# Optimization experiments

Hardware: AMD Instinct MI355X
Metric: run time of the kernel (lower is better)

Reference implementation:

```python
import jax, jax.numpy as jnp
import numpy as np

N_NODES = 100000
N_EDGES = 1600000
DIM_IN = 128
DIM_OUT = 128


def setup_inputs() -> dict:
    key = jax.random.key(0)
    k1, k2, k3, k4, k5 = jax.random.split(key, 5)
    x = jax.random.normal(k1, (N_NODES, DIM_IN), dtype=jnp.float32)
    W = jax.random.normal(k2, (DIM_OUT, DIM_IN), dtype=jnp.float32) * (1.0 / np.sqrt(DIM_IN))
    vals = jax.random.uniform(k3, (N_EDGES,), dtype=jnp.float32)
    src = jax.random.randint(k4, (N_EDGES,), 0, N_NODES, dtype=jnp.int32)
    dst = jax.random.randint(k5, (N_EDGES,), 0, N_NODES, dtype=jnp.int32)
    return {"x": x, "W": W, "vals": vals, "src": src, "dst": dst}


def reference(x, W, vals, src, dst):
    # Linear projection (nn.Linear with bias=False): h = x @ W^T  -> [N, dim_out]
    h = jnp.einsum('nd,od->no', x, W)
    # Sparse adjacency SpMM in COO form: out[i] = sum_{e: dst[e]==i} vals[e] * h[src[e]]
    msgs = vals[:, None] * h[src]  # [E, dim_out] irregular gather
    out = jax.ops.segment_sum(msgs, dst, num_segments=N_NODES)  # [N, dim_out] scatter-add
    return out
```

## Files before the change

kernel.cpp:

```cpp
#include <hip/hip_runtime.h>

#define N_NODES 100000
#define N_EDGES 1600000
#define DIM 128

#define NPB 64
#define NBUCK 1563
#define EPB 2048
#define NBLK_E 782
#define NBLK_G 1563

#define OFF_H       0
#define OFF_BCNT    25600000
#define OFF_BBASE   25606272
#define OFF_BCUR    25612544
#define OFF_EPACK   25618816
#define OFF_ROWPTR  38418816
#define WS_NEED     38818944

typedef __attribute__((ext_vector_type(8))) __bf16 bf16x8;
typedef __attribute__((ext_vector_type(4))) float  f32x4;

union U4B8 { uint4 u; bf16x8 v; };
union S8B8 { unsigned short s[8]; bf16x8 v; };

static __device__ __forceinline__ unsigned short f2bf(float f) {
    union { float f; unsigned u; } a; a.f = f;
    unsigned r = a.u + 0x7fffu + ((a.u >> 16) & 1u);
    return (unsigned short)(r >> 16);
}

static __device__ __forceinline__ float bf2f(unsigned short h) {
    return __uint_as_float((unsigned)h << 16);
}

static __device__ __forceinline__ float bflo(unsigned b) {
    return __uint_as_float(b << 16);
}
static __device__ __forceinline__ float bfhi(unsigned b) {
    return __uint_as_float(b & 0xffff0000u);
}

__global__ __launch_bounds__(256) void zero_out_kernel(float4* __restrict__ out) {
    int i = blockIdx.x * 256 + threadIdx.x;
    if (i < N_NODES * DIM / 4) out[i] = make_float4(0.f, 0.f, 0.f, 0.f);
}

__global__ __launch_bounds__(256) void zero_bcnt_kernel(int* __restrict__ c) {
    int i = blockIdx.x * 256 + threadIdx.x;
    if (i < NBUCK) c[i] = 0;
}

#define GMR 64
__global__ __launch_bounds__(256) void gemm_mfma_kernel(
        const float4* __restrict__ x4,
        const float4* __restrict__ W4,
        unsigned short* __restrict__ hb16)
{
    __shared__ alignas(16) unsigned whi[128 * 64];
    __shared__ alignas(16) unsigned wlo[128 * 64];

    const int t    = threadIdx.x;
    const int lane = t & 63;
    const int w    = t >> 6;
    const int r0   = blockIdx.x * GMR;

#pragma unroll
    for (int i = 0; i < 16; ++i) {
        int idx = t + 256 * i;
        int j   = idx >> 5;
        int c4  = idx & 31;
        float4 v = W4[idx];
        unsigned short hx = f2bf(v.x), hy = f2bf(v.y);
        unsigned short hz = f2bf(v.z), hw = f2bf(v.w);
        unsigned short lx = f2bf(v.x - bf2f(hx));
        unsigned short ly = f2bf(v.y - bf2f(hy));
        unsigned short lz = f2bf(v.z - bf2f(hz));
        unsigned short lw = f2bf(v.w - bf2f(hw));
        int d = c4 * 2;
        int p = d ^ ((j & 7) << 2);
        int base = j * 64;
        whi[base + p]     = (unsigned)hx | ((unsigned)hy << 16);
        whi[base + p + 1] = (unsigned)hz | ((unsigned)hw << 16);
        wlo[base + p]     = (unsigned)lx | ((unsigned)ly << 16);
        wlo[base + p + 1] = (unsigned)lz | ((unsigned)lw << 16);
    }
    __syncthreads();

    const int arow = r0 + (w << 4) + (lane & 15);
    const bool rok = arow < N_NODES;
    const int kg   = lane >> 4;

    f32x4 acc[8];
#pragma unroll
    for (int jt = 0; jt < 8; ++jt) acc[jt] = (f32x4)(0.f);

#pragma unroll
    for (int ks = 0; ks < 4; ++ks) {
        float4 a0 = make_float4(0.f, 0.f, 0.f, 0.f);
        float4 a1 = make_float4(0.f, 0.f, 0.f, 0.f);
        if (rok) {
            a0 = x4[(size_t)arow * 32 + ks * 8 + kg * 2];
            a1 = x4[(size_t)arow * 32 + ks * 8 + kg * 2 + 1];
        }
        float av[8] = {a0.x, a0.y, a0.z, a0.w, a1.x, a1.y, a1.z, a1.w};
        S8B8 ahi, alo;
#pragma unroll
        for (int e = 0; e < 8; ++e) {
            unsigned short h = f2bf(av[e]);
            ahi.s[e] = h;
            alo.s[e] = f2bf(av[e] - bf2f(h));
        }

        const int d0 = (ks << 4) + (kg << 2);
#pragma unroll
        for (int jt = 0; jt < 8; ++jt) {
            int j  = (jt << 4) + (lane & 15);
            int p0 = d0 ^ ((j & 7) << 2);
            U4B8 bh, bl;
            bh.u = *(const uint4*)&whi[j * 64 + p0];
            bl.u = *(const uint4*)&wlo[j * 64 + p0];
            acc[jt] = __builtin_amdgcn_mfma_f32_16x16x32_bf16(ahi.v, bh.v, acc[jt], 0, 0, 0);
            acc[jt] = __builtin_amdgcn_mfma_f32_16x16x32_bf16(alo.v, bh.v, acc[jt], 0, 0, 0);
            acc[jt] = __builtin_amdgcn_mfma_f32_16x16x32_bf16(ahi.v, bl.v, acc[jt], 0, 0, 0);
        }
    }

#pragma unroll
    for (int jt = 0; jt < 8; ++jt) {
#pragma unroll
        for (int r = 0; r < 4; ++r) {
            int node = r0 + (w << 4) + kg * 4 + r;
            if (node < N_NODES)
                hb16[(size_t)node * 128 + (jt << 4) + (lane & 15)] = f2bf(acc[jt][r]);
        }
    }
}

__global__ __launch_bounds__(256) void bucket_hist_kernel(
        const int* __restrict__ dst, int* __restrict__ bcnt)
{
    __shared__ int lh[NBUCK];
    const int t = threadIdx.x;
    const int e0 = blockIdx.x * EPB;

    for (int i = t; i < NBUCK; i += 256) lh[i] = 0;
    __syncthreads();
#pragma unroll
    for (int r = 0; r < 8; ++r) {
        int e = e0 + (r << 8) + t;
        if (e < N_EDGES) atomicAdd(&lh[dst[e] >> 6], 1);
    }
    __syncthreads();
    const int phase = (blockIdx.x * 613) % NBUCK;
    for (int k = t; k < NBUCK; k += 256) {
        int i = k + phase; if (i >= NBUCK) i -= NBUCK;
        int c = lh[i];
        if (c) atomicAdd(&bcnt[i], c);
    }
}

__global__ __launch_bounds__(256) void bucket_scan_kernel(
        const int* __restrict__ bcnt, int* __restrict__ bbase,
        int* __restrict__ bcur)
{
    __shared__ int wsh[4];
    const int t = threadIdx.x, lane = t & 63, wv = t >> 6;
    int c[8]; int s = 0;
#pragma unroll
    for (int i = 0; i < 8; ++i) {
        int idx = t * 8 + i;
        c[i] = (idx < NBUCK) ? bcnt[idx] : 0;
        s += c[i];
    }
    int v = s;
#pragma unroll
    for (int off = 1; off < 64; off <<= 1) {
        int u = __shfl_up(v, off, 64);
        if (lane >= off) v += u;
    }
    if (lane == 63) wsh[wv] = v;
    __syncthreads();
    int we = 0;
#pragma unroll
    for (int w = 0; w < 4; ++w) we += (w < wv) ? wsh[w] : 0;
    int run = we + (v - s);
#pragma unroll
    for (int i = 0; i < 8; ++i) {
        int idx = t * 8 + i;
        if (idx < NBUCK) { bbase[idx] = run; bcur[idx] = run; }
        run += c[i];
    }
    if (t == 0) bbase[NBUCK] = N_EDGES;
}

__global__ __launch_bounds__(256) void bucket_fill_kernel(
        const int* __restrict__ src, const int* __restrict__ dst,
        const float* __restrict__ vals,
        int* __restrict__ bcur, uint2* __restrict__ ep)
{
    __shared__ int lh[NBUCK];
    __shared__ int lbase[NBUCK];
    const int t = threadIdx.x;
    const int e0 = blockIdx.x * EPB;

    for (int i = t; i < NBUCK; i += 256) lh[i] = 0;
    __syncthreads();
#pragma unroll
    for (int r = 0; r < 8; ++r) {
        int e = e0 + (r << 8) + t;
        if (e < N_EDGES) atomicAdd(&lh[dst[e] >> 6], 1);
    }
    __syncthreads();
    const int phase = (blockIdx.x * 613) % NBUCK;
    for (int k = t; k < NBUCK; k += 256) {
        int i = k + phase; if (i >= NBUCK) i -= NBUCK;
        int c = lh[i];
        lbase[i] = c ? atomicAdd(&bcur[i], c) : 0;
        lh[i] = 0;
    }
    __syncthreads();
#pragma unroll
    for (int r = 0; r < 8; ++r) {
        int e = e0 + (r << 8) + t;
        if (e < N_EDGES) {
            int d  = dst[e];
            int bk = d >> 6;
            int p  = lbase[bk] + atomicAdd(&lh[bk], 1);
            ep[p] = make_uint2((unsigned)src[e] | ((unsigned)(d & 63) << 17),
                               __float_as_uint(vals[e]));
        }
    }
}

__global__ __launch_bounds__(256) void reorder_kernel(
        const int* __restrict__ bbase,
        uint2* __restrict__ ep,
        int* __restrict__ row_ptr)
{
    __shared__ int lcnt[NPB];
    const int t = threadIdx.x;
    const int lane = t & 63;
    const int wv = t >> 6;
    const int b = blockIdx.x;

    const int jb = bbase[b];
    const int je = bbase[b + 1];
    const int cnt = je - jb;

    uint2 e[8];
#pragma unroll
    for (int r = 0; r < 8; ++r) {
        int idx = t + (r << 8);
        if (idx < cnt) e[r] = ep[jb + idx];
    }
    if (t < NPB) lcnt[t] = 0;
    __syncthreads();
#pragma unroll
    for (int r = 0; r < 8; ++r) {
        int idx = t + (r << 8);
        if (idx < cnt) atomicAdd(&lcnt[e[r].x >> 17], 1);
    }
    __syncthreads();
    if (wv == 0) {
        int c = lcnt[lane];
        int v = c;
#pragma unroll
        for (int off = 1; off < 64; off <<= 1) {
            int u = __shfl_up(v, off, 64);
            if (lane >= off) v += u;
        }
        int excl = v - c;
        lcnt[lane] = excl;
        int node = b * NPB + lane;
        if (node <= N_NODES) row_ptr[node] = jb + excl;
    }
    __syncthreads();
#pragma unroll
    for (int r = 0; r < 8; ++r) {
        int idx = t + (r << 8);
        if (idx < cnt) {
            int p = atomicAdd(&lcnt[e[r].x >> 17], 1);
            ep[jb + p] = make_uint2(e[r].x & 0x1FFFFu, e[r].y);
        }
    }
}

__global__ __launch_bounds__(256) void gather_bf16_kernel(
        const unsigned int* __restrict__ hbits,
        const int* __restrict__ row_ptr,
        const uint2* __restrict__ ep,
        float2* __restrict__ out2)
{
    const int lane = threadIdx.x & 63;
    const int node = blockIdx.x * 4 + (threadIdx.x >> 6);
    if (node >= N_NODES) return;

    const int jb = row_ptr[node];
    const int je = row_ptr[node + 1];

    float ax0 = 0.f, ay0 = 0.f, ax1 = 0.f, ay1 = 0.f;
    float ax2 = 0.f, ay2 = 0.f, ax3 = 0.f, ay3 = 0.f;
    float ax4 = 0.f, ay4 = 0.f, ax5 = 0.f, ay5 = 0.f;
    float ax6 = 0.f, ay6 = 0.f, ax7 = 0.f, ay7 = 0.f;

    int j = jb;
    if ((j & 1) && j < je) {
        uint2 e0 = ep[j];
        unsigned b0 = hbits[((size_t)e0.x << 6) + lane];
        float v0 = __uint_as_float(e0.y);
        ax0 += v0 * bflo(b0);
        ay0 += v0 * bfhi(b0);
        ++j;
    }
    for (; j + 7 < je; j += 8) {
        uint4 q0 = *(const uint4*)(ep + j);
        uint4 q1 = *(const uint4*)(ep + j + 2);
        uint4 q2 = *(const uint4*)(ep + j + 4);
        uint4 q3 = *(const uint4*)(ep + j + 6);
        unsigned b0 = hbits[((size_t)q0.x << 6) + lane];
        unsigned b1 = hbits[((size_t)q0.z << 6) + lane];
        unsigned b2 = hbits[((size_t)q1.x << 6) + lane];
        unsigned b3 = hbits[((size_t)q1.z << 6) + lane];
        unsigned b4 = hbits[((size_t)q2.x << 6) + lane];
        unsigned b5 = hbits[((size_t)q2.z << 6) + lane];
        unsigned b6 = hbits[((size_t)q3.x << 6) + lane];
        unsigned b7 = hbits[((size_t)q3.z << 6) + lane];
        float v0 = __uint_as_float(q0.y), v1 = __uint_as_float(q0.w);
        float v2 = __uint_as_float(q1.y), v3 = __uint_as_float(q1.w);
        float v4 = __uint_as_float(q2.y), v5 = __uint_as_float(q2.w);
        float v6 = __uint_as_float(q3.y), v7 = __uint_as_float(q3.w);
        ax0 += v0 * bflo(b0); ay0 += v0 * bfhi(b0);
        ax1 += v1 * bflo(b1); ay1 += v1 * bfhi(b1);
        ax2 += v2 * bflo(b2); ay2 += v2 * bfhi(b2);
        ax3 += v3 * bflo(b3); ay3 += v3 * bfhi(b3);
        ax4 += v4 * bflo(b4); ay4 += v4 * bfhi(b4);
        ax5 += v5 * bflo(b5); ay5 += v5 * bfhi(b5);
        ax6 += v6 * bflo(b6); ay6 += v6 * bfhi(b6);
        ax7 += v7 * bflo(b7); ay7 += v7 * bfhi(b7);
    }
    for (; j + 1 < je; j += 2) {
        uint4 q0 = *(const uint4*)(ep + j);
        unsigned b0 = hbits[((size_t)q0.x << 6) + lane];
        unsigned b1 = hbits[((size_t)q0.z << 6) + lane];
        float v0 = __uint_as_float(q0.y), v1 = __uint_as_float(q0.w);
        ax0 += v0 * bflo(b0); ay0 += v0 * bfhi(b0);
        ax1 += v1 * bflo(b1); ay1 += v1 * bfhi(b1);
    }
    if (j < je) {
        uint2 e0 = ep[j];
        unsigned b0 = hbits[((size_t)e0.x << 6) + lane];
        float v0 = __uint_as_float(e0.y);
        ax0 += v0 * bflo(b0);
        ay0 += v0 * bfhi(b0);
    }
    float sx = ((ax0 + ax1) + (ax2 + ax3)) + ((ax4 + ax5) + (ax6 + ax7));
    float sy = ((ay0 + ay1) + (ay2 + ay3)) + ((ay4 + ay5) + (ay6 + ay7));
    out2[(size_t)node * 64 + lane] = make_float2(sx, sy);
}

#define GR 64
__global__ __launch_bounds__(256) void gemm_tiled_kernel(
        const float4* __restrict__ x4, const float4* __restrict__ W4,
        unsigned int* __restrict__ hbits)
{
    __shared__ alignas(16) float xs[GR][68];
    __shared__ alignas(16) float wsh[64][132];

    const int t  = threadIdx.x;
    const int tx = t & 15;
    const int ty = t >> 4;
    const int r0 = blockIdx.x * GR;

    float acc[4][8];
#pragma unroll
    for (int i = 0; i < 4; ++i)
#pragma unroll
        for (int j = 0; j < 8; ++j) acc[i][j] = 0.f;

    for (int kc = 0; kc < 2; ++kc) {
#pragma unroll
        for (int i = 0; i < 4; ++i) {
            int linear = t + 256 * i;
            int r  = linear >> 4;
            int k4 = linear & 15;
            float4 v = make_float4(0.f, 0.f, 0.f, 0.f);
            if (r0 + r < N_NODES) v = x4[(size_t)(r0 + r) * 32 + kc * 16 + k4];
            *(float4*)&xs[r][k4 * 4] = v;
        }
#pragma unroll
        for (int i = 0; i < 8; ++i) {
            int linear = t + 256 * i;
            int c  = linear >> 4;
            int k4 = linear & 15;
            float4 v = W4[(size_t)c * 32 + kc * 16 + k4];
            wsh[k4 * 4 + 0][c] = v.x;
            wsh[k4 * 4 + 1][c] = v.y;
            wsh[k4 * 4 + 2][c] = v.z;
            wsh[k4 * 4 + 3][c] = v.w;
        }
        __syncthreads();
#pragma unroll 4
        for (int kk = 0; kk < 64; ++kk) {
            float xf[4], wf[8];
#pragma unroll
            for (int i = 0; i < 4; ++i) xf[i] = xs[ty * 4 + i][kk];
            float4 wlo4 = *(const float4*)&wsh[kk][tx * 8];
            float4 whi4 = *(const float4*)&wsh[kk][tx * 8 + 4];
            wf[0] = wlo4.x; wf[1] = wlo4.y; wf[2] = wlo4.z; wf[3] = wlo4.w;
            wf[4] = whi4.x; wf[5] = whi4.y; wf[6] = whi4.z; wf[7] = whi4.w;
#pragma unroll
            for (int i = 0; i < 4; ++i)
#pragma unroll
                for (int j = 0; j < 8; ++j) acc[i][j] += xf[i] * wf[j];
        }
        __syncthreads();
    }
#pragma unroll
    for (int i = 0; i < 4; ++i) {
        int r = r0 + ty * 4 + i;
        if (r < N_NODES) {
            uint4 u;
            u.x = (unsigned)f2bf(acc[i][0]) | ((unsigned)f2bf(acc[i][1]) << 16);
            u.y = (unsigned)f2bf(acc[i][2]) | ((unsigned)f2bf(acc[i][3]) << 16);
            u.z = (unsigned)f2bf(acc[i][4]) | ((unsigned)f2bf(acc[i][5]) << 16);
            u.w = (unsigned)f2bf(acc[i][6]) | ((unsigned)f2bf(acc[i][7]) << 16);
            *(uint4*)&hbits[(size_t)r * 64 + tx * 4] = u;
        }
    }
}

__global__ __launch_bounds__(256) void scatter_kernel(
        const unsigned int* __restrict__ hbits, const float* __restrict__ vals,
        const int* __restrict__ src, const int* __restrict__ dst,
        float* __restrict__ out)
{
    const int lane = threadIdx.x & 63;
    int e = (blockIdx.x * 256 + threadIdx.x) >> 6;
    if (e >= N_EDGES) return;
    const int   s = src[e];
    const int   d = dst[e];
    const float v = vals[e];
    unsigned b = hbits[(size_t)s * 64 + lane];
    float* op = out + (size_t)d * DIM + lane * 2;
    atomicAdd(op + 0, v * bflo(b));
    atomicAdd(op + 1, v * bfhi(b));
}

extern "C" void kernel_launch(void* const* d_in, const int* in_sizes, int n_in,
                              void* d_out, int out_size, void* d_ws, size_t ws_size,
                              hipStream_t stream) {
    const float* x    = (const float*)d_in[0];
    const float* W    = (const float*)d_in[1];
    const float* vals = (const float*)d_in[2];
    const int*   src  = (const int*)d_in[3];
    const int*   dst  = (const int*)d_in[4];
    float* out = (float*)d_out;

    char* ws = (char*)d_ws;
    unsigned* hbits = (unsigned*)(ws + OFF_H);
    int*   bcnt    = (int*)(ws + OFF_BCNT);
    int*   bbase   = (int*)(ws + OFF_BBASE);
    int*   bcur    = (int*)(ws + OFF_BCUR);
    uint2* ep      = (uint2*)(ws + OFF_EPACK);
    int*   row_ptr = (int*)(ws + OFF_ROWPTR);

    if (ws_size >= (size_t)WS_NEED) {
        zero_bcnt_kernel<<<(NBUCK + 255) / 256, 256, 0, stream>>>(bcnt);
        bucket_hist_kernel<<<NBLK_E, 256, 0, stream>>>(dst, bcnt);
        bucket_scan_kernel<<<1, 256, 0, stream>>>(bcnt, bbase, bcur);
        gemm_mfma_kernel<<<NBLK_G, 256, 0, stream>>>(
            (const float4*)x, (const float4*)W, (unsigned short*)hbits);
        bucket_fill_kernel<<<NBLK_E, 256, 0, stream>>>(src, dst, vals, bcur, ep);
        reorder_kernel<<<NBUCK, 256, 0, stream>>>(bbase, ep, row_ptr);
        gather_bf16_kernel<<<(N_NODES + 3) / 4, 256, 0, stream>>>(
            hbits, row_ptr, ep, (float2*)out);
    } else {
        gemm_tiled_kernel<<<NBLK_G, 256, 0, stream>>>(
            (const float4*)x, (const float4*)W, hbits);
        zero_out_kernel<<<(N_NODES * DIM / 4 + 255) / 256, 256, 0, stream>>>((float4*)out);
        scatter_kernel<<<(N_EDGES * 64 + 255) / 256, 256, 0, stream>>>(
            hbits, vals, src, dst, out);
    }
}
```

Baseline: 289.0 us.

## Precompute split-bf16 W once and double GEMM row tile per block

A new prep kernel converts W into hi/lo bf16 planes in a pre-swizzled global layout once and also zeroes the bucket counters, replacing the per-block conversion in every GEMM block. The GEMM now handles 128 rows per block with two row tiles sharing each W fragment load, and stages W in two K-chunks so it uses half the LDS. The bucket histogram and fill kernels process 4096 edges per block, which halves the block count and the global atomic merges. In exchange, registers per thread rise with the doubled accumulators, the extra syncs may cost occupancy, and there are fewer, larger blocks.

```diff
diff --git a/kernel.cpp b/kernel.cpp
--- a/kernel.cpp
+++ b/kernel.cpp
@@ -6,9 +6,10 @@
 
 #define NPB 64
 #define NBUCK 1563
-#define EPB 2048
-#define NBLK_E 782
+#define EPB 4096
+#define NBLK_E 391
 #define NBLK_G 1563
+#define NBLK_M 782
 
 #define OFF_H       0
 #define OFF_BCNT    25600000
@@ -16,13 +17,14 @@
 #define OFF_BCUR    25612544
 #define OFF_EPACK   25618816
 #define OFF_ROWPTR  38418816
-#define WS_NEED     38818944
+#define OFF_WPL     38818944
+#define WS_NEED     38884480
 
 typedef __attribute__((ext_vector_type(8))) __bf16 bf16x8;
 typedef __attribute__((ext_vector_type(4))) float  f32x4;
 
 union U4B8 { uint4 u; bf16x8 v; };
-union S8B8 { unsigned short s[8]; bf16x8 v; };
+union B8   { __bf16 b[8]; bf16x8 v; };
 
 static __device__ __forceinline__ unsigned short f2bf(float f) {
     union { float f; unsigned u; } a; a.f = f;
@@ -46,28 +48,13 @@
     if (i < N_NODES * DIM / 4) out[i] = make_float4(0.f, 0.f, 0.f, 0.f);
 }
 
-__global__ __launch_bounds__(256) void zero_bcnt_kernel(int* __restrict__ c) {
-    int i = blockIdx.x * 256 + threadIdx.x;
-    if (i < NBUCK) c[i] = 0;
-}
-
-#define GMR 64
-__global__ __launch_bounds__(256) void gemm_mfma_kernel(
-        const float4* __restrict__ x4,
-        const float4* __restrict__ W4,
-        unsigned short* __restrict__ hb16)
-{
-    __shared__ alignas(16) unsigned whi[128 * 64];
-    __shared__ alignas(16) unsigned wlo[128 * 64];
-
-    const int t    = threadIdx.x;
-    const int lane = t & 63;
-    const int w    = t >> 6;
-    const int r0   = blockIdx.x * GMR;
-
-#pragma unroll
-    for (int i = 0; i < 16; ++i) {
-        int idx = t + 256 * i;
+__global__ __launch_bounds__(256) void prep_kernel(
+        const float4* __restrict__ W4, unsigned* __restrict__ wpl,
+        int* __restrict__ bcnt)
+{
+    const int b = blockIdx.x;
+    if (b < 16) {
+        int idx = b * 256 + threadIdx.x;
         int j   = idx >> 5;
         int c4  = idx & 31;
         float4 v = W4[idx];
@@ -77,62 +64,107 @@
         unsigned short ly = f2bf(v.y - bf2f(hy));
         unsigned short lz = f2bf(v.z - bf2f(hz));
         unsigned short lw = f2bf(v.w - bf2f(hw));
-        int d = c4 * 2;
-        int p = d ^ ((j & 7) << 2);
-        int base = j * 64;
-        whi[base + p]     = (unsigned)hx | ((unsigned)hy << 16);
-        whi[base + p + 1] = (unsigned)hz | ((unsigned)hw << 16);
-        wlo[base + p]     = (unsigned)lx | ((unsigned)ly << 16);
-        wlo[base + p + 1] = (unsigned)lz | ((unsigned)lw << 16);
-    }
-    __syncthreads();
-
-    const int arow = r0 + (w << 4) + (lane & 15);
-    const bool rok = arow < N_NODES;
+        int dg = c4 * 2;
+        int kc = dg >> 5;
+        int dl = dg & 31;
+        int p  = dl ^ ((j & 7) << 2);
+        int base = kc * 8192 + j * 32;
+        wpl[base + p]            = (unsigned)hx | ((unsigned)hy << 16);
+        wpl[base + p + 1]        = (unsigned)hz | ((unsigned)hw << 16);
+        wpl[base + 4096 + p]     = (unsigned)lx | ((unsigned)ly << 16);
+        wpl[base + 4096 + p + 1] = (unsigned)lz | ((unsigned)lw << 16);
+    } else {
+        int i = (b - 16) * 256 + threadIdx.x;
+        if (i < NBUCK) bcnt[i] = 0;
+    }
+}
+
+#define GMR 128
+__global__ __launch_bounds__(256) void gemm_mfma_kernel(
+        const float4* __restrict__ x4,
+        const unsigned* __restrict__ wpl,
+        unsigned short* __restrict__ hb16)
+{
+    __shared__ alignas(16) unsigned lw[8192];
+
+    const int t    = threadIdx.x;
+    const int lane = t & 63;
+    const int w    = t >> 6;
+    const int col  = lane & 15;
     const int kg   = lane >> 4;
-
-    f32x4 acc[8];
-#pragma unroll
-    for (int jt = 0; jt < 8; ++jt) acc[jt] = (f32x4)(0.f);
-
-#pragma unroll
-    for (int ks = 0; ks < 4; ++ks) {
-        float4 a0 = make_float4(0.f, 0.f, 0.f, 0.f);
-        float4 a1 = make_float4(0.f, 0.f, 0.f, 0.f);
-        if (rok) {
-            a0 = x4[(size_t)arow * 32 + ks * 8 + kg * 2];
-            a1 = x4[(size_t)arow * 32 + ks * 8 + kg * 2 + 1];
-        }
-        float av[8] = {a0.x, a0.y, a0.z, a0.w, a1.x, a1.y, a1.z, a1.w};
-        S8B8 ahi, alo;
-#pragma unroll
-        for (int e = 0; e < 8; ++e) {
-            unsigned short h = f2bf(av[e]);
-            ahi.s[e] = h;
-            alo.s[e] = f2bf(av[e] - bf2f(h));
-        }
-
-        const int d0 = (ks << 4) + (kg << 2);
+    const int r0   = blockIdx.x * GMR;
+
+    const int arow0 = r0 + (w << 4) + col;
+    const int arow1 = arow0 + 64;
+    const bool ok0 = arow0 < N_NODES;
+    const bool ok1 = arow1 < N_NODES;
+
+    f32x4 acc[2][8];
+#pragma unroll
+    for (int rt = 0; rt < 2; ++rt)
+#pragma unroll
+        for (int jt = 0; jt < 8; ++jt) acc[rt][jt] = (f32x4)(0.f);
+
+    for (int kc = 0; kc < 2; ++kc) {
+        const uint4* g = (const uint4*)(wpl + kc * 8192);
+#pragma unroll
+        for (int i = 0; i < 8; ++i)
+            ((uint4*)lw)[t + 256 * i] = g[t + 256 * i];
+        __syncthreads();
+
+#pragma unroll
+        for (int kh = 0; kh < 2; ++kh) {
+            const int ks = kc * 2 + kh;
+
+            B8 ah[2], al[2];
+#pragma unroll
+            for (int rt = 0; rt < 2; ++rt) {
+                float4 a0 = make_float4(0.f, 0.f, 0.f, 0.f);
+                float4 a1 = make_float4(0.f, 0.f, 0.f, 0.f);
+                const int arow = rt ? arow1 : arow0;
+                const bool ok  = rt ? ok1 : ok0;
+                if (ok) {
+                    a0 = x4[(size_t)arow * 32 + ks * 8 + kg * 2];
+                    a1 = x4[(size_t)arow * 32 + ks * 8 + kg * 2 + 1];
+                }
+                float av[8] = {a0.x, a0.y, a0.z, a0.w, a1.x, a1.y, a1.z, a1.w};
+#pragma unroll
+                for (int e = 0; e < 8; ++e) {
+                    __bf16 h = (__bf16)av[e];
+                    ah[rt].b[e] = h;
+                    al[rt].b[e] = (__bf16)(av[e] - (float)h);
+                }
+            }
+
+            const int d0 = (kh << 4) + (kg << 2);
+#pragma unroll
+            for (int jt = 0; jt < 8; ++jt) {
+                int j  = (jt << 4) + col;
+                int p0 = d0 ^ ((j & 7) << 2);
+                U4B8 bh, bl;
+                bh.u = *(const uint4*)&lw[j * 32 + p0];
+                bl.u = *(const uint4*)&lw[4096 + j * 32 + p0];
+                acc[0][jt] = __builtin_amdgcn_mfma_f32_16x16x32_bf16(ah[0].v, bh.v, acc[0][jt], 0, 0, 0);
+                acc[0][jt] = __builtin_amdgcn_mfma_f32_16x16x32_bf16(al[0].v, bh.v, acc[0][jt], 0, 0, 0);
+                acc[0][jt] = __builtin_amdgcn_mfma_f32_16x16x32_bf16(ah[0].v, bl.v, acc[0][jt], 0, 0, 0);
+                acc[1][jt] = __builtin_amdgcn_mfma_f32_16x16x32_bf16(ah[1].v, bh.v, acc[1][jt], 0, 0, 0);
+                acc[1][jt] = __builtin_amdgcn_mfma_f32_16x16x32_bf16(al[1].v, bh.v, acc[1][jt], 0, 0, 0);
+                acc[1][jt] = __builtin_amdgcn_mfma_f32_16x16x32_bf16(ah[1].v, bl.v, acc[1][jt], 0, 0, 0);
+            }
+        }
+        __syncthreads();
+    }
+
+#pragma unroll
+    for (int rt = 0; rt < 2; ++rt) {
 #pragma unroll
         for (int jt = 0; jt < 8; ++jt) {
-            int j  = (jt << 4) + (lane & 15);
-            int p0 = d0 ^ ((j & 7) << 2);
-            U4B8 bh, bl;
-            bh.u = *(const uint4*)&whi[j * 64 + p0];
-            bl.u = *(const uint4*)&wlo[j * 64 + p0];
-            acc[jt] = __builtin_amdgcn_mfma_f32_16x16x32_bf16(ahi.v, bh.v, acc[jt], 0, 0, 0);
-            acc[jt] = __builtin_amdgcn_mfma_f32_16x16x32_bf16(alo.v, bh.v, acc[jt], 0, 0, 0);
-            acc[jt] = __builtin_amdgcn_mfma_f32_16x16x32_bf16(ahi.v, bl.v, acc[jt], 0, 0, 0);
-        }
-    }
-
-#pragma unroll
-    for (int jt = 0; jt < 8; ++jt) {
-#pragma unroll
-        for (int r = 0; r < 4; ++r) {
-            int node = r0 + (w << 4) + kg * 4 + r;
-            if (node < N_NODES)
-                hb16[(size_t)node * 128 + (jt << 4) + (lane & 15)] = f2bf(acc[jt][r]);
+#pragma unroll
+            for (int r = 0; r < 4; ++r) {
+                int node = r0 + rt * 64 + (w << 4) + kg * 4 + r;
+                if (node < N_NODES)
+                    hb16[(size_t)node * 128 + (jt << 4) + col] = f2bf(acc[rt][jt][r]);
+            }
         }
     }
 }
@@ -147,7 +179,7 @@
     for (int i = t; i < NBUCK; i += 256) lh[i] = 0;
     __syncthreads();
 #pragma unroll
-    for (int r = 0; r < 8; ++r) {
+    for (int r = 0; r < 16; ++r) {
         int e = e0 + (r << 8) + t;
         if (e < N_EDGES) atomicAdd(&lh[dst[e] >> 6], 1);
     }
@@ -207,7 +239,7 @@
     for (int i = t; i < NBUCK; i += 256) lh[i] = 0;
     __syncthreads();
 #pragma unroll
-    for (int r = 0; r < 8; ++r) {
+    for (int r = 0; r < 16; ++r) {
         int e = e0 + (r << 8) + t;
         if (e < N_EDGES) atomicAdd(&lh[dst[e] >> 6], 1);
     }
@@ -221,7 +253,7 @@
     }
     __syncthreads();
 #pragma unroll
-    for (int r = 0; r < 8; ++r) {
+    for (int r = 0; r < 16; ++r) {
         int e = e0 + (r << 8) + t;
         if (e < N_EDGES) {
             int d  = dst[e];
@@ -464,13 +496,14 @@
     int*   bcur    = (int*)(ws + OFF_BCUR);
     uint2* ep      = (uint2*)(ws + OFF_EPACK);
     int*   row_ptr = (int*)(ws + OFF_ROWPTR);
+    unsigned* wpl  = (unsigned*)(ws + OFF_WPL);
 
     if (ws_size >= (size_t)WS_NEED) {
-        zero_bcnt_kernel<<<(NBUCK + 255) / 256, 256, 0, stream>>>(bcnt);
+        prep_kernel<<<16 + 7, 256, 0, stream>>>((const float4*)W, wpl, bcnt);
         bucket_hist_kernel<<<NBLK_E, 256, 0, stream>>>(dst, bcnt);
         bucket_scan_kernel<<<1, 256, 0, stream>>>(bcnt, bbase, bcur);
-        gemm_mfma_kernel<<<NBLK_G, 256, 0, stream>>>(
-            (const float4*)x, (const float4*)W, (unsigned short*)hbits);
+        gemm_mfma_kernel<<<NBLK_M, 256, 0, stream>>>(
+            (const float4*)x, wpl, (unsigned short*)hbits);
         bucket_fill_kernel<<<NBLK_E, 256, 0, stream>>>(src, dst, vals, bcur, ep);
         reorder_kernel<<<NBUCK, 256, 0, stream>>>(bbase, ep, row_ptr);
         gather_bf16_kernel<<<(N_NODES + 3) / 4, 256, 0, stream>>>(
```

Measured after the change: 269.3 us. 1.07x faster.
